# Kernel tuning notes

Measured on AMD Instinct MI355X. Metric: run time of the kernel, lower is better.

## Reference

```python
import jax, jax.numpy as jnp
import numpy as np

WINDOW = 11
C1 = 0.01 ** 2
C2 = 0.03 ** 2
PAD = WINDOW // 2


def _box_filter(img, kernel):
    # img: [B,1,H,W], kernel: [1,1,w,w]; SAME padding (odd window)
    return jax.lax.conv_general_dilated(
        img, kernel,
        window_strides=(1, 1),
        padding=[(PAD, PAD), (PAD, PAD)],
        dimension_numbers=('NCHW', 'OIHW', 'NCHW'))


def setup_inputs() -> dict:
    key = jax.random.key(0)
    kx, ky = jax.random.split(key)
    B, C, H, W = 64, 1, 512, 512
    x = jax.random.uniform(kx, (B, C, H, W), dtype=jnp.float32)
    y = jax.random.uniform(ky, (B, C, H, W), dtype=jnp.float32)
    kernel = jnp.ones((1, 1, WINDOW, WINDOW), dtype=jnp.float32) / (WINDOW ** 2)
    return {"x": x, "y": y, "kernel": kernel}


def reference(x, y, kernel):
    mu_x = _box_filter(x, kernel)
    mu_y = _box_filter(y, kernel)
    mu_x2 = mu_x * mu_x
    mu_y2 = mu_y * mu_y
    mu_xy = mu_x * mu_y
    sigma_x2 = _box_filter(x * x, kernel) - mu_x2
    sigma_y2 = _box_filter(y * y, kernel) - mu_y2
    sigma_xy = _box_filter(x * y, kernel) - mu_xy
    ssim_map = ((2.0 * mu_xy + C1) * (2.0 * sigma_xy + C2)) / (
        (mu_x2 + mu_y2 + C1) * (sigma_x2 + sigma_y2 + C2))
    return 1.0 - jnp.mean(ssim_map)
```

## Files before the change

### kernel.cpp

```cpp
#include <hip/hip_runtime.h>
#include <stdint.h>


#define IMG_H 512
#define IMG_W 512
#define N_IMG 64
#define BAND  32
#define NBANDG 16
#define NBLOCKS (N_IMG * NBANDG)

#define C1S2 1.4641f
#define C2S2 13.1769f

__device__ __forceinline__ float dpp_shr1(float v) {
    return __int_as_float(__builtin_amdgcn_update_dpp(
        0, __float_as_int(v), 0x138, 0xF, 0xF, true));
}
__device__ __forceinline__ float dpp_shl1(float v) {
    return __int_as_float(__builtin_amdgcn_update_dpp(
        0, __float_as_int(v), 0x130, 0xF, 0xF, true));
}

__global__ __launch_bounds__(64) void ssim_fused(const float* __restrict__ x,
                                                 const float* __restrict__ y,
                                                 float* __restrict__ part)
{
    const int tx = threadIdx.x;
    const int wid = (blockIdx.x & 7) * (NBLOCKS / 8) + (blockIdx.x >> 3);
    const int img = wid >> 4;
    const int bg  = wid & (NBANDG - 1);
    const int r0  = bg * BAND;
    const int c0  = tx * 8;

    const float* __restrict__ xi = x + (size_t)img * (IMG_H * IMG_W) + c0;
    const float* __restrict__ yi = y + (size_t)img * (IMG_H * IMG_W) + c0;

    float X[12][8], Y[12][8];
    float Vx[8], Vy[8], Vss[8], Vxy[8];
#pragma unroll
    for (int j = 0; j < 8; ++j) { Vx[j] = 0.f; Vy[j] = 0.f; Vss[j] = 0.f; Vxy[j] = 0.f; }

#define LOADROW(u, rowv) do {                                             \
        int rc_ = (rowv);                                                 \
        rc_ = rc_ < 0 ? 0 : (rc_ > IMG_H - 1 ? IMG_H - 1 : rc_);          \
        const float4* px_ = (const float4*)(xi + (size_t)rc_ * IMG_W);    \
        const float4* py_ = (const float4*)(yi + (size_t)rc_ * IMG_W);    \
        float4 a_ = px_[0], b_ = px_[1];                                  \
        float4 c_ = py_[0], d_ = py_[1];                                  \
        X[u][0] = a_.x; X[u][1] = a_.y; X[u][2] = a_.z; X[u][3] = a_.w;   \
        X[u][4] = b_.x; X[u][5] = b_.y; X[u][6] = b_.z; X[u][7] = b_.w;   \
        Y[u][0] = c_.x; Y[u][1] = c_.y; Y[u][2] = c_.z; Y[u][3] = c_.w;   \
        Y[u][4] = d_.x; Y[u][5] = d_.y; Y[u][6] = d_.z; Y[u][7] = d_.w;   \
    } while (0)

#define ADDS(s) do { _Pragma("unroll")                                    \
        for (int j = 0; j < 8; ++j) {                                     \
            Vx[j] += X[s][j];                                             \
            Vy[j] += Y[s][j];                                             \
            Vss[j] = fmaf(X[s][j], X[s][j], Vss[j]);                      \
            Vss[j] = fmaf(Y[s][j], Y[s][j], Vss[j]);                      \
            Vxy[j] = fmaf(X[s][j], Y[s][j], Vxy[j]);                      \
        } } while (0)

#define SUBS(s) do { _Pragma("unroll")                                    \
        for (int j = 0; j < 8; ++j) {                                     \
            Vx[j] -= X[s][j];                                             \
            Vy[j] -= Y[s][j];                                             \
            Vss[j] = fmaf(-X[s][j], X[s][j], Vss[j]);                     \
            Vss[j] = fmaf(-Y[s][j], Y[s][j], Vss[j]);                     \
            Vxy[j] = fmaf(-X[s][j], Y[s][j], Vxy[j]);                     \
        } } while (0)

    auto hsum = [&](const float (&V)[8], float (&S)[8]) {
        float w[18];
#pragma unroll
        for (int k = 0; k < 5; ++k) w[k] = dpp_shr1(V[3 + k]);
#pragma unroll
        for (int j = 0; j < 8; ++j) w[5 + j] = V[j];
#pragma unroll
        for (int k = 0; k < 5; ++k) w[13 + k] = dpp_shl1(V[k]);
        float s0 = (w[0] + w[1]) + (w[2] + w[3]);
        float s1 = (w[4] + w[5]) + (w[6] + w[7]);
        float s2 = (w[8] + w[9]) + w[10];
        float s  = (s0 + s1) + s2;
        S[0] = s;
#pragma unroll
        for (int j = 1; j < 8; ++j) { s += w[j + 10] - w[j - 1]; S[j] = s; }
    };

    float loss = 0.0f;

#define SSIM8() do { _Pragma("unroll")                                    \
        for (int j = 0; j < 8; ++j) {                                     \
            float A  = Sx[j] * Sy[j];                                     \
            float B  = fmaf(Sx[j], Sx[j], Sy[j] * Sy[j]);                 \
            float n1 = fmaf(A, 2.0f, C1S2);                               \
            float n2 = fmaf(Sxy[j], 242.0f, fmaf(A, -2.0f, C2S2));        \
            float d1 = B + C1S2;                                          \
            float d2 = fmaf(Sss[j], 121.0f, C2S2 - B);                    \
            loss += __fdividef(n1 * n2, d1 * d2);                         \
        } } while (0)

#define STEP(u) do {                                                      \
        const int r_ = rb + (u);                                          \
        if (r_ - 6 >= 0) SUBS(u);                                         \
        LOADROW(u, r_ + 6);                                               \
        if (r_ + 5 < IMG_H) ADDS(((u) + 11) % 12);                        \
        float Sx[8], Sy[8], Sss[8], Sxy[8];                               \
        hsum(Vx, Sx); hsum(Vy, Sy); hsum(Vss, Sss); hsum(Vxy, Sxy);       \
        SSIM8();                                                          \
    } while (0)

#pragma unroll
    for (int k = 0; k < 12; ++k) LOADROW(k, r0 - 6 + k);
#pragma unroll
    for (int k = 0; k < 11; ++k) {
        if (r0 - 6 + k >= 0) ADDS(k);
    }

#pragma unroll 1
    for (int g = 0; g < 2; ++g) {
        const int rb = r0 + 12 * g;
        STEP(0);  STEP(1);  STEP(2);  STEP(3);
        STEP(4);  STEP(5);  STEP(6);  STEP(7);
        STEP(8);  STEP(9);  STEP(10); STEP(11);
    }
    {
        const int rb = r0 + 24;
        STEP(0); STEP(1); STEP(2); STEP(3);
        STEP(4); STEP(5); STEP(6); STEP(7);
    }

#pragma unroll
    for (int off = 32; off > 0; off >>= 1)
        loss += __shfl_down(loss, off, 64);
    if (tx == 0)
        atomicAdd(&part[blockIdx.x & 511], loss);
}

__global__ __launch_bounds__(256) void ssim_reduce(const float* __restrict__ part,
                                                   float* __restrict__ out)
{
    const int t  = threadIdx.x;
    const int tx = t & 63;
    float s = part[t] + part[t + 256];
#pragma unroll
    for (int off = 32; off > 0; off >>= 1)
        s += __shfl_down(s, off, 64);
    __shared__ float ws[4];
    if (tx == 0) ws[t >> 6] = s;
    __syncthreads();
    if (t == 0) {
        float total = (ws[0] + ws[1]) + (ws[2] + ws[3]);
        out[0] = 1.0f - total * (1.0f / ((float)N_IMG * IMG_H * IMG_W));
    }
}

extern "C" void kernel_launch(void* const* d_in, const int* in_sizes, int n_in,
                              void* d_out, int out_size, void* d_ws, size_t ws_size,
                              hipStream_t stream) {
    const float* x = (const float*)d_in[0];
    const float* y = (const float*)d_in[1];
    float* part = (float*)d_ws;

    hipMemsetAsync(part, 0, 512 * sizeof(float), stream);
    ssim_fused<<<NBLOCKS, 64, 0, stream>>>(x, y, part);
    ssim_reduce<<<1, 256, 0, stream>>>(part, (float*)d_out);
}
```

Before: 191.5 us.

## Replace 12-row register ring with re-loaded trailing rows and halve band height

Result: faster. 179.2 us (-6.4%).

```diff
diff --git a/kernel.cpp b/kernel.cpp
--- a/kernel.cpp
+++ b/kernel.cpp
@@ -5,8 +5,8 @@
 #define IMG_H 512
 #define IMG_W 512
 #define N_IMG 64
-#define BAND  32
-#define NBANDG 16
+#define BAND  16
+#define NBANDG 32
 #define NBLOCKS (N_IMG * NBANDG)
 
 #define C1S2 1.4641f
@@ -27,7 +27,7 @@
 {
     const int tx = threadIdx.x;
     const int wid = (blockIdx.x & 7) * (NBLOCKS / 8) + (blockIdx.x >> 3);
-    const int img = wid >> 4;
+    const int img = wid >> 5;
     const int bg  = wid & (NBANDG - 1);
     const int r0  = bg * BAND;
     const int c0  = tx * 8;
@@ -35,40 +35,41 @@
     const float* __restrict__ xi = x + (size_t)img * (IMG_H * IMG_W) + c0;
     const float* __restrict__ yi = y + (size_t)img * (IMG_H * IMG_W) + c0;
 
-    float X[12][8], Y[12][8];
     float Vx[8], Vy[8], Vss[8], Vxy[8];
 #pragma unroll
     for (int j = 0; j < 8; ++j) { Vx[j] = 0.f; Vy[j] = 0.f; Vss[j] = 0.f; Vxy[j] = 0.f; }
 
-#define LOADROW(u, rowv) do {                                             \
+    float Ax[8], Ay[8], Bx[8], By[8], Cx[8], Cy[8];
+
+#define LOADR(PX, PY, rowv) do {                                          \
         int rc_ = (rowv);                                                 \
         rc_ = rc_ < 0 ? 0 : (rc_ > IMG_H - 1 ? IMG_H - 1 : rc_);          \
         const float4* px_ = (const float4*)(xi + (size_t)rc_ * IMG_W);    \
         const float4* py_ = (const float4*)(yi + (size_t)rc_ * IMG_W);    \
         float4 a_ = px_[0], b_ = px_[1];                                  \
         float4 c_ = py_[0], d_ = py_[1];                                  \
-        X[u][0] = a_.x; X[u][1] = a_.y; X[u][2] = a_.z; X[u][3] = a_.w;   \
-        X[u][4] = b_.x; X[u][5] = b_.y; X[u][6] = b_.z; X[u][7] = b_.w;   \
-        Y[u][0] = c_.x; Y[u][1] = c_.y; Y[u][2] = c_.z; Y[u][3] = c_.w;   \
-        Y[u][4] = d_.x; Y[u][5] = d_.y; Y[u][6] = d_.z; Y[u][7] = d_.w;   \
+        PX[0]=a_.x; PX[1]=a_.y; PX[2]=a_.z; PX[3]=a_.w;                   \
+        PX[4]=b_.x; PX[5]=b_.y; PX[6]=b_.z; PX[7]=b_.w;                   \
+        PY[0]=c_.x; PY[1]=c_.y; PY[2]=c_.z; PY[3]=c_.w;                   \
+        PY[4]=d_.x; PY[5]=d_.y; PY[6]=d_.z; PY[7]=d_.w;                   \
     } while (0)
 
-#define ADDS(s) do { _Pragma("unroll")                                    \
+#define ADD8(PX, PY) do { _Pragma("unroll")                               \
         for (int j = 0; j < 8; ++j) {                                     \
-            Vx[j] += X[s][j];                                             \
-            Vy[j] += Y[s][j];                                             \
-            Vss[j] = fmaf(X[s][j], X[s][j], Vss[j]);                      \
-            Vss[j] = fmaf(Y[s][j], Y[s][j], Vss[j]);                      \
-            Vxy[j] = fmaf(X[s][j], Y[s][j], Vxy[j]);                      \
+            Vx[j] += PX[j];                                               \
+            Vy[j] += PY[j];                                               \
+            Vss[j] = fmaf(PX[j], PX[j], Vss[j]);                          \
+            Vss[j] = fmaf(PY[j], PY[j], Vss[j]);                          \
+            Vxy[j] = fmaf(PX[j], PY[j], Vxy[j]);                          \
         } } while (0)
 
-#define SUBS(s) do { _Pragma("unroll")                                    \
+#define SUB8(PX, PY) do { _Pragma("unroll")                               \
         for (int j = 0; j < 8; ++j) {                                     \
-            Vx[j] -= X[s][j];                                             \
-            Vy[j] -= Y[s][j];                                             \
-            Vss[j] = fmaf(-X[s][j], X[s][j], Vss[j]);                     \
-            Vss[j] = fmaf(-Y[s][j], Y[s][j], Vss[j]);                     \
-            Vxy[j] = fmaf(-X[s][j], Y[s][j], Vxy[j]);                     \
+            Vx[j] -= PX[j];                                               \
+            Vy[j] -= PY[j];                                               \
+            Vss[j] = fmaf(-PX[j], PX[j], Vss[j]);                         \
+            Vss[j] = fmaf(-PY[j], PY[j], Vss[j]);                         \
+            Vxy[j] = fmaf(-PX[j], PY[j], Vxy[j]);                         \
         } } while (0)
 
     auto hsum = [&](const float (&V)[8], float (&S)[8]) {
@@ -92,43 +93,50 @@
 
 #define SSIM8() do { _Pragma("unroll")                                    \
         for (int j = 0; j < 8; ++j) {                                     \
-            float A  = Sx[j] * Sy[j];                                     \
-            float B  = fmaf(Sx[j], Sx[j], Sy[j] * Sy[j]);                 \
-            float n1 = fmaf(A, 2.0f, C1S2);                               \
-            float n2 = fmaf(Sxy[j], 242.0f, fmaf(A, -2.0f, C2S2));        \
-            float d1 = B + C1S2;                                          \
-            float d2 = fmaf(Sss[j], 121.0f, C2S2 - B);                    \
-            loss += __fdividef(n1 * n2, d1 * d2);                         \
+            float A_  = Sx[j] * Sy[j];                                    \
+            float B_  = fmaf(Sx[j], Sx[j], Sy[j] * Sy[j]);                \
+            float n1_ = fmaf(A_, 2.0f, C1S2);                             \
+            float n2_ = fmaf(Sxy[j], 242.0f, fmaf(A_, -2.0f, C2S2));      \
+            float d1_ = B_ + C1S2;                                        \
+            float d2_ = fmaf(Sss[j], 121.0f, C2S2 - B_);                  \
+            loss += __fdividef(n1_ * n2_, d1_ * d2_);                     \
         } } while (0)
 
-#define STEP(u) do {                                                      \
-        const int r_ = rb + (u);                                          \
-        if (r_ - 6 >= 0) SUBS(u);                                         \
-        LOADROW(u, r_ + 6);                                               \
-        if (r_ + 5 < IMG_H) ADDS(((u) + 11) % 12);                        \
-        float Sx[8], Sy[8], Sss[8], Sxy[8];                               \
-        hsum(Vx, Sx); hsum(Vy, Sy); hsum(Vss, Sss); hsum(Vxy, Sxy);       \
-        SSIM8();                                                          \
-    } while (0)
-
-#pragma unroll
-    for (int k = 0; k < 12; ++k) LOADROW(k, r0 - 6 + k);
-#pragma unroll
-    for (int k = 0; k < 11; ++k) {
-        if (r0 - 6 + k >= 0) ADDS(k);
-    }
+    LOADR(Ax, Ay, r0 - 5);
+    LOADR(Bx, By, r0 - 4);
+#define WARM2(k)                                                          \
+    if (r0 - 5 + (k) >= 0) ADD8(Ax, Ay);                                  \
+    LOADR(Ax, Ay, r0 - 3 + (k));                                          \
+    if (r0 - 4 + (k) >= 0) ADD8(Bx, By);                                  \
+    LOADR(Bx, By, r0 - 2 + (k));
+    WARM2(0) WARM2(2) WARM2(4) WARM2(6)
+    if (r0 + 3 >= 0) ADD8(Ax, Ay);
+    LOADR(Ax, Ay, r0 + 5);
+    ADD8(Bx, By);
+#undef WARM2
 
 #pragma unroll 1
-    for (int g = 0; g < 2; ++g) {
-        const int rb = r0 + 12 * g;
-        STEP(0);  STEP(1);  STEP(2);  STEP(3);
-        STEP(4);  STEP(5);  STEP(6);  STEP(7);
-        STEP(8);  STEP(9);  STEP(10); STEP(11);
-    }
-    {
-        const int rb = r0 + 24;
-        STEP(0); STEP(1); STEP(2); STEP(3);
-        STEP(4); STEP(5); STEP(6); STEP(7);
+    for (int i = 0; i < BAND; i += 2) {
+        const int r = r0 + i;
+        LOADR(Cx, Cy, r - 5);
+        LOADR(Bx, By, r + 6);
+        if (r + 5 < IMG_H) ADD8(Ax, Ay);
+        {
+            float Sx[8], Sy[8], Sss[8], Sxy[8];
+            hsum(Vx, Sx); hsum(Vy, Sy); hsum(Vss, Sss); hsum(Vxy, Sxy);
+            SSIM8();
+        }
+        if (r - 5 >= 0) SUB8(Cx, Cy);
+
+        LOADR(Cx, Cy, r - 4);
+        LOADR(Ax, Ay, r + 7);
+        if (r + 6 < IMG_H) ADD8(Bx, By);
+        {
+            float Sx[8], Sy[8], Sss[8], Sxy[8];
+            hsum(Vx, Sx); hsum(Vy, Sy); hsum(Vss, Sss); hsum(Vxy, Sxy);
+            SSIM8();
+        }
+        if (r - 4 >= 0) SUB8(Cx, Cy);
     }
 
 #pragma unroll
```
